# Optimization experiments

Measured on AMD Instinct MI355X. Metric: run time of the kernel, lower is better.

Reference implementation:

```python
import math
import jax, jax.numpy as jnp
import numpy as np

DIM = 1024
QK_DIM = 200
HIDDEN = 2 * DIM  # expansion_factor = 2
N = 8192


def setup_inputs() -> dict:
    key = jax.random.key(0)
    ks = jax.random.split(key, 8)
    s = 0.02
    return {
        "x": jax.random.normal(ks[0], (N, DIM), dtype=jnp.float32),
        "W_hidden": jax.random.normal(ks[1], (DIM, 2 * HIDDEN), dtype=jnp.float32) * s,
        "b_hidden": jnp.zeros((2 * HIDDEN,), dtype=jnp.float32),
        "W_qk": jax.random.normal(ks[2], (DIM, QK_DIM), dtype=jnp.float32) * s,
        "b_qk": jnp.zeros((QK_DIM,), dtype=jnp.float32),
        "gamma": 1.0 + jax.random.normal(ks[3], (2, QK_DIM), dtype=jnp.float32) * s,
        "beta": jnp.zeros((2, QK_DIM), dtype=jnp.float32),
        "W_out": jax.random.normal(ks[4], (HIDDEN, DIM), dtype=jnp.float32) * s,
        "b_out": jnp.zeros((DIM,), dtype=jnp.float32),
    }


def reference(x, W_hidden, b_hidden, W_qk, b_qk, gamma, beta, W_out, b_out):
    # to_hidden: Linear(dim -> 2*hidden) + SiLU, then chunk into v, gate
    hid = jax.nn.silu(x @ W_hidden + b_hidden)        # [N, 2H]
    v, gate = jnp.split(hid, 2, axis=-1)              # [N, H] each
    # to_qk: Linear(dim -> qk_dim) + SiLU
    qk = jax.nn.silu(x @ W_qk + b_qk)                 # [N, qk]
    # OffsetScale (heads=2): per-head affine on the shared qk
    q = qk * gamma[0] + beta[0]                       # [N, qk]
    k = qk * gamma[1] + beta[1]                       # [N, qk]
    # scores scaled by sqrt(dim) (module uses self.dim, not qk_dim)
    sim = (q @ k.T) * (1.0 / math.sqrt(x.shape[-1]))  # [N, N]
    # ReLU-squared attention (no softmax); dropout=0.0 -> identity
    attn = jnp.square(jax.nn.relu(sim))
    out = attn @ v                                    # [N, H]
    out = out * gate
    out = out @ W_out + b_out                         # [N, dim]
    # add_residual=True in this module multiplies by x
    return out * x
```

## Files before the change

kernel.cpp:

```cpp
#include <hip/hip_runtime.h>
#include <stdint.h>


typedef __bf16 bf16x8 __attribute__((ext_vector_type(8)));
typedef float f32x4 __attribute__((ext_vector_type(4)));

__device__ __forceinline__ uint16_t f2bf(float f) {
  uint32_t u = __builtin_bit_cast(uint32_t, f);
  u += 0x7fffu + ((u >> 16) & 1u);
  return (uint16_t)(u >> 16);
}
__device__ __forceinline__ float bf2f(uint16_t h) {
  uint32_t u = ((uint32_t)h) << 16;
  return __builtin_bit_cast(float, u);
}
__device__ __forceinline__ float silu_f(float s) {
  return s / (1.f + __expf(-s));
}

__device__ __forceinline__ void gload16(const void* g, void* l) {
  __builtin_amdgcn_global_load_lds(
      (__attribute__((address_space(1))) void*)const_cast<void*>(g),
      (__attribute__((address_space(3))) void*)l, 16, 0, 0);
}


__global__ void cast_to_bf16(const float* __restrict__ in, uint16_t* __restrict__ out, int n4) {
  int i = blockIdx.x * blockDim.x + threadIdx.x;
  if (i < n4) {
    float4 f = ((const float4*)in)[i];
    ushort4 o;
    o.x = f2bf(f.x); o.y = f2bf(f.y); o.z = f2bf(f.z); o.w = f2bf(f.w);
    ((ushort4*)out)[i] = o;
  }
}

__global__ void transpose_cast_pad(const float* __restrict__ in, uint16_t* __restrict__ out,
                                   int R, int C, int Cp) {
  __shared__ float tile[32][33];
  int cb = blockIdx.x * 32;
  int rb = blockIdx.y * 32;
  int tx = threadIdx.x;
  int ty = threadIdx.y;
#pragma unroll
  for (int i = 0; i < 4; ++i) {
    int r = rb + ty + i * 8;
    int c = cb + tx;
    tile[ty + i * 8][tx] = (c < C) ? in[(size_t)r * C + c] : 0.f;
  }
  __syncthreads();
#pragma unroll
  for (int i = 0; i < 4; ++i) {
    int c = cb + ty + i * 8;
    if (c < Cp) out[(size_t)c * R + rb + tx] = f2bf(tile[tx][ty + i * 8]);
  }
}


struct EpiParams {
  const float* bias;
  const float* g0;
  const float* b0;
  const float* g1;
  const float* b1;
  const uint16_t* gate;
  const float* x;
  uint16_t* o16a;
  uint16_t* o16b;
  float* o32;
};

template <int MODE>
__global__ __launch_bounds__(256) void gemm_bt(
    const uint16_t* __restrict__ A, int lda,
    const uint16_t* __restrict__ Bt, int ldb,
    int K, EpiParams p) {
  __shared__ __align__(16) uint16_t As[128 * 32];
  __shared__ __align__(16) uint16_t Bs[128 * 32];

  const int tid = threadIdx.x;
  const int lane = tid & 63;
  const int wave = tid >> 6;
  const int wr = (wave >> 1) * 64;
  const int wc = (wave & 1) * 64;
  const int m0 = blockIdx.y * 128;
  const int n0 = blockIdx.x * 128;

  f32x4 acc[4][4] = {};

  const int r0 = tid >> 2;
  const int q8 = (tid & 3) * 8;
  const uint16_t* gA0 = A + (size_t)(m0 + r0) * lda + q8;
  const uint16_t* gA1 = A + (size_t)(m0 + 64 + r0) * lda + q8;
  const uint16_t* gB0 = Bt + (size_t)(n0 + r0) * ldb + q8;
  const uint16_t* gB1 = Bt + (size_t)(n0 + 64 + r0) * ldb + q8;
  uint16_t* lA0 = As + wave * 512;
  uint16_t* lA1 = As + 2048 + wave * 512;
  uint16_t* lB0 = Bs + wave * 512;
  uint16_t* lB1 = Bs + 2048 + wave * 512;

  const int fr = lane & 15;
  const int kq = (lane >> 4) * 8;

  for (int k0 = 0; k0 < K; k0 += 32) {
    __syncthreads();
    gload16(gA0 + k0, lA0);
    gload16(gA1 + k0, lA1);
    gload16(gB0 + k0, lB0);
    gload16(gB1 + k0, lB1);
    __syncthreads();

    bf16x8 a[4], b[4];
#pragma unroll
    for (int i = 0; i < 4; ++i)
      a[i] = *(const bf16x8*)(As + (wr + i * 16 + fr) * 32 + kq);
#pragma unroll
    for (int j = 0; j < 4; ++j)
      b[j] = *(const bf16x8*)(Bs + (wc + j * 16 + fr) * 32 + kq);
#pragma unroll
    for (int i = 0; i < 4; ++i)
#pragma unroll
      for (int j = 0; j < 4; ++j)
        acc[i][j] = __builtin_amdgcn_mfma_f32_16x16x32_bf16(a[i], b[j], acc[i][j], 0, 0, 0);
  }

#pragma unroll
  for (int i = 0; i < 4; ++i) {
#pragma unroll
    for (int j = 0; j < 4; ++j) {
      const int row = m0 + wr + i * 16 + (lane >> 4) * 4;
      const int col = n0 + wc + j * 16 + fr;

      if constexpr (MODE == 0) {
        const float bc = p.bias[col];
        if (col < 2048) {
          ushort4 o;
          float s0 = silu_f(acc[i][j][0] + bc);
          float s1 = silu_f(acc[i][j][1] + bc);
          float s2 = silu_f(acc[i][j][2] + bc);
          float s3 = silu_f(acc[i][j][3] + bc);
          o.x = f2bf(s0); o.y = f2bf(s1); o.z = f2bf(s2); o.w = f2bf(s3);
          *(ushort4*)(p.o16a + (size_t)col * 8192 + row) = o;
        } else {
#pragma unroll
          for (int r = 0; r < 4; ++r) {
            float s = silu_f(acc[i][j][r] + bc);
            p.o16b[(size_t)(row + r) * 2048 + (col - 2048)] = f2bf(s);
          }
        }
      } else if constexpr (MODE == 1) {
        if (col < 224) {
#pragma unroll
          for (int r = 0; r < 4; ++r) {
            float qv = 0.f, kv = 0.f;
            if (col < 200) {
              float s = silu_f(acc[i][j][r] + p.bias[col]);
              qv = s * p.g0[col] + p.b0[col];
              kv = s * p.g1[col] + p.b1[col];
            }
            p.o16a[(size_t)(row + r) * 224 + col] = f2bf(qv);
            p.o16b[(size_t)(row + r) * 224 + col] = f2bf(kv);
          }
        }
      } else if constexpr (MODE == 2) {
#pragma unroll
        for (int r = 0; r < 4; ++r) {
          float s = acc[i][j][r] * 0.03125f;
          s = fmaxf(s, 0.f);
          p.o16a[(size_t)(row + r) * 8192 + col] = f2bf(s * s);
        }
      } else {
        const float bc = p.bias[col];
#pragma unroll
        for (int r = 0; r < 4; ++r) {
          size_t idx = (size_t)(row + r) * 1024 + col;
          p.o32[idx] = (acc[i][j][r] + bc) * p.x[idx];
        }
      }
    }
  }
}

__global__ __launch_bounds__(512) void gemm_wide3(
    const uint16_t* __restrict__ A, int lda,
    const uint16_t* __restrict__ Bt, int ldb,
    int K, int nx, EpiParams p) {
  __shared__ __align__(16) uint16_t As[128 * 32];
  __shared__ __align__(16) uint16_t Bs[256 * 32];

  const int id = blockIdx.x;
  const int bx = (id >> 3) % nx;
  const int by = (id & 7) + 8 * (id / (8 * nx));
  const int m0 = by * 128;
  const int n0 = bx * 256;

  const int tid = threadIdx.x;
  const int lane = tid & 63;
  const int wave = tid >> 6;
  const int wr = (wave & 1) * 64;
  const int wc = (wave >> 1) * 64;

  f32x4 acc[4][4] = {};

  const int r0 = tid >> 2;
  const int q8 = (tid & 3) * 8;
  const uint16_t* gA  = A  + (size_t)(m0 + r0) * lda + q8;
  const uint16_t* gB0 = Bt + (size_t)(n0 + r0) * ldb + q8;
  const uint16_t* gB1 = Bt + (size_t)(n0 + 128 + r0) * ldb + q8;
  uint16_t* lA  = As + wave * 512;
  uint16_t* lB0 = Bs + wave * 512;
  uint16_t* lB1 = Bs + 4096 + wave * 512;

  const int fr = lane & 15;
  const int kq = (lane >> 4) * 8;

  for (int k0 = 0; k0 < K; k0 += 32) {
    __syncthreads();
    gload16(gA + k0, lA);
    gload16(gB0 + k0, lB0);
    gload16(gB1 + k0, lB1);
    __syncthreads();

    bf16x8 a[4], b[4];
#pragma unroll
    for (int i = 0; i < 4; ++i)
      a[i] = *(const bf16x8*)(As + (wr + i * 16 + fr) * 32 + kq);
#pragma unroll
    for (int j = 0; j < 4; ++j)
      b[j] = *(const bf16x8*)(Bs + (wc + j * 16 + fr) * 32 + kq);
#pragma unroll
    for (int i = 0; i < 4; ++i)
#pragma unroll
      for (int j = 0; j < 4; ++j)
        acc[i][j] = __builtin_amdgcn_mfma_f32_16x16x32_bf16(a[i], b[j], acc[i][j], 0, 0, 0);
  }

#pragma unroll
  for (int i = 0; i < 4; ++i) {
#pragma unroll
    for (int j = 0; j < 4; ++j) {
      const int row = m0 + wr + i * 16 + (lane >> 4) * 4;
      const int col = n0 + wc + j * 16 + fr;
#pragma unroll
      for (int r = 0; r < 4; ++r) {
        float g = bf2f(p.gate[(size_t)(row + r) * 2048 + col]);
        p.o16a[(size_t)(row + r) * 2048 + col] = f2bf(acc[i][j][r] * g);
      }
    }
  }
}


extern "C" void kernel_launch(void* const* d_in, const int* in_sizes, int n_in,
                              void* d_out, int out_size, void* d_ws, size_t ws_size,
                              hipStream_t stream) {
  const float* x        = (const float*)d_in[0];
  const float* W_hidden = (const float*)d_in[1];
  const float* b_hidden = (const float*)d_in[2];
  const float* W_qk     = (const float*)d_in[3];
  const float* b_qk     = (const float*)d_in[4];
  const float* gamma    = (const float*)d_in[5];
  const float* beta     = (const float*)d_in[6];
  const float* W_out    = (const float*)d_in[7];
  const float* b_out    = (const float*)d_in[8];
  float* out = (float*)d_out;

  const bool fullM = ws_size >= (236ull << 20);
  const size_t region0 = fullM ? (128ull << 20) : (64ull << 20);

  char* base = (char*)d_ws;
  uint16_t* xb    = (uint16_t*)(base);
  uint16_t* WhT   = (uint16_t*)(base + (16ull << 20));
  uint16_t* WqkT  = (uint16_t*)(base + (24ull << 20));
  uint16_t* attnB = (uint16_t*)(base);
  char* tail = base + region0;
  uint16_t* WoT   = (uint16_t*)(tail);
  uint16_t* q     = (uint16_t*)(tail + (4ull << 20));
  uint16_t* kk    = (uint16_t*)(tail + (4ull << 20) + 3670016);
  uint16_t* vT    = (uint16_t*)(tail + (4ull << 20) + 2 * 3670016);
  uint16_t* gate  = (uint16_t*)(tail + (4ull << 20) + 2 * 3670016 + (32ull << 20));
  uint16_t* out2g = (uint16_t*)(tail + (4ull << 20) + 2 * 3670016 + (64ull << 20));
  (void)in_sizes; (void)n_in; (void)out_size;

  cast_to_bf16<<<(8192 * 1024 / 4) / 256, 256, 0, stream>>>(x, xb, 8192 * 1024 / 4);
  transpose_cast_pad<<<dim3(4096 / 32, 1024 / 32), dim3(32, 8), 0, stream>>>(W_hidden, WhT, 1024, 4096, 4096);
  transpose_cast_pad<<<dim3(256 / 32, 1024 / 32), dim3(32, 8), 0, stream>>>(W_qk, WqkT, 1024, 200, 256);
  transpose_cast_pad<<<dim3(1024 / 32, 2048 / 32), dim3(32, 8), 0, stream>>>(W_out, WoT, 2048, 1024, 1024);

  {
    EpiParams p{};
    p.bias = b_qk; p.g0 = gamma; p.b0 = beta; p.g1 = gamma + 200; p.b1 = beta + 200;
    p.o16a = q; p.o16b = kk;
    gemm_bt<1><<<dim3(2, 64), 256, 0, stream>>>(xb, 1024, WqkT, 1024, 1024, p);
  }
  {
    EpiParams p{};
    p.bias = b_hidden; p.o16a = vT; p.o16b = gate;
    gemm_bt<0><<<dim3(32, 64), 256, 0, stream>>>(xb, 1024, WhT, 1024, 1024, p);
  }

  if (fullM) {
    {
      EpiParams p{};
      p.o16a = attnB;
      gemm_bt<2><<<dim3(64, 64), 256, 0, stream>>>(q, 224, kk, 224, 224, p);
    }
    {
      EpiParams p{};
      p.gate = gate; p.o16a = out2g;
      gemm_wide3<<<dim3(8 * 64), 512, 0, stream>>>(attnB, 8192, vT, 8192, 8192, 8, p);
    }
  } else {
    for (int s = 0; s < 2; ++s) {
      {
        EpiParams p{};
        p.o16a = attnB;
        gemm_bt<2><<<dim3(64, 32), 256, 0, stream>>>(q + (size_t)s * 4096 * 224, 224, kk, 224, 224, p);
      }
      {
        EpiParams p{};
        p.gate = gate + (size_t)s * 4096 * 2048;
        p.o16a = out2g + (size_t)s * 4096 * 2048;
        gemm_wide3<<<dim3(8 * 32), 512, 0, stream>>>(attnB, 8192, vT, 8192, 8192, 8, p);
      }
    }
  }

  {
    EpiParams p{};
    p.bias = b_out; p.x = x; p.o32 = out;
    gemm_bt<4><<<dim3(8, 64), 256, 0, stream>>>(out2g, 2048, WoT, 2048, 2048, p);
  }
}
```

Before: 668.6 us.

## Fuse hidden and qk projections, coalesce attention score stores via LDS staging

The hidden and qk projection GEMMs become one launch over 34 column tiles. The extra tiles read the WqkT buffer that sits directly after WhT in the workspace, so the two weight matrices act as one concatenated matrix. The score kernel's epilogue now stages each wave's ReLU-squared bf16 tile in shared memory, then writes it as 16-byte vector rows instead of scattered 2-byte stores. This targets the large score matrix write. Kernels are also specialised with constant K and strides. The cost is extra LDS use in the score kernel, and the fusion relies on WqkT being contiguous with WhT.

```diff
diff --git a/kernel.cpp b/kernel.cpp
--- a/kernel.cpp
+++ b/kernel.cpp
@@ -59,6 +59,7 @@
 
 struct EpiParams {
   const float* bias;
+  const float* bias2;
   const float* g0;
   const float* b0;
   const float* g1;
@@ -67,14 +68,13 @@
   const float* x;
   uint16_t* o16a;
   uint16_t* o16b;
+  uint16_t* oq;
+  uint16_t* ok;
   float* o32;
 };
 
-template <int MODE>
-__global__ __launch_bounds__(256) void gemm_bt(
-    const uint16_t* __restrict__ A, int lda,
-    const uint16_t* __restrict__ Bt, int ldb,
-    int K, EpiParams p) {
+__global__ __launch_bounds__(256) void k_fused_hid_qk(
+    const uint16_t* __restrict__ A, const uint16_t* __restrict__ Bt, EpiParams p) {
   __shared__ __align__(16) uint16_t As[128 * 32];
   __shared__ __align__(16) uint16_t Bs[128 * 32];
 
@@ -85,6 +85,7 @@
   const int wc = (wave & 1) * 64;
   const int m0 = blockIdx.y * 128;
   const int n0 = blockIdx.x * 128;
+  const int lda = 1024, ldb = 1024, K = 1024;
 
   f32x4 acc[4][4] = {};
 
@@ -131,57 +132,115 @@
       const int row = m0 + wr + i * 16 + (lane >> 4) * 4;
       const int col = n0 + wc + j * 16 + fr;
 
-      if constexpr (MODE == 0) {
+      if (col < 2048) {
         const float bc = p.bias[col];
-        if (col < 2048) {
-          ushort4 o;
-          float s0 = silu_f(acc[i][j][0] + bc);
-          float s1 = silu_f(acc[i][j][1] + bc);
-          float s2 = silu_f(acc[i][j][2] + bc);
-          float s3 = silu_f(acc[i][j][3] + bc);
-          o.x = f2bf(s0); o.y = f2bf(s1); o.z = f2bf(s2); o.w = f2bf(s3);
-          *(ushort4*)(p.o16a + (size_t)col * 8192 + row) = o;
-        } else {
+        ushort4 o;
+        o.x = f2bf(silu_f(acc[i][j][0] + bc));
+        o.y = f2bf(silu_f(acc[i][j][1] + bc));
+        o.z = f2bf(silu_f(acc[i][j][2] + bc));
+        o.w = f2bf(silu_f(acc[i][j][3] + bc));
+        *(ushort4*)(p.o16a + (size_t)col * 8192 + row) = o;
+      } else if (col < 4096) {
+        const float bc = p.bias[col];
+#pragma unroll
+        for (int r = 0; r < 4; ++r)
+          p.o16b[(size_t)(row + r) * 2048 + (col - 2048)] = f2bf(silu_f(acc[i][j][r] + bc));
+      } else {
+        const int qc = col - 4096;
+        if (qc < 224) {
 #pragma unroll
           for (int r = 0; r < 4; ++r) {
-            float s = silu_f(acc[i][j][r] + bc);
-            p.o16b[(size_t)(row + r) * 2048 + (col - 2048)] = f2bf(s);
+            float qv = 0.f, kv = 0.f;
+            if (qc < 200) {
+              float s = silu_f(acc[i][j][r] + p.bias2[qc]);
+              qv = s * p.g0[qc] + p.b0[qc];
+              kv = s * p.g1[qc] + p.b1[qc];
+            }
+            p.oq[(size_t)(row + r) * 224 + qc] = f2bf(qv);
+            p.ok[(size_t)(row + r) * 224 + qc] = f2bf(kv);
           }
         }
-      } else if constexpr (MODE == 1) {
-        if (col < 224) {
-#pragma unroll
-          for (int r = 0; r < 4; ++r) {
-            float qv = 0.f, kv = 0.f;
-            if (col < 200) {
-              float s = silu_f(acc[i][j][r] + p.bias[col]);
-              qv = s * p.g0[col] + p.b0[col];
-              kv = s * p.g1[col] + p.b1[col];
-            }
-            p.o16a[(size_t)(row + r) * 224 + col] = f2bf(qv);
-            p.o16b[(size_t)(row + r) * 224 + col] = f2bf(kv);
-          }
-        }
-      } else if constexpr (MODE == 2) {
-#pragma unroll
-        for (int r = 0; r < 4; ++r) {
-          float s = acc[i][j][r] * 0.03125f;
-          s = fmaxf(s, 0.f);
-          p.o16a[(size_t)(row + r) * 8192 + col] = f2bf(s * s);
-        }
-      } else {
-        const float bc = p.bias[col];
-#pragma unroll
-        for (int r = 0; r < 4; ++r) {
-          size_t idx = (size_t)(row + r) * 1024 + col;
-          p.o32[idx] = (acc[i][j][r] + bc) * p.x[idx];
-        }
-      }
-    }
-  }
-}
-
-__global__ __launch_bounds__(512) void gemm_wide3(
+      }
+    }
+  }
+}
+
+__global__ __launch_bounds__(256) void k_attn(
+    const uint16_t* __restrict__ A,
+    const uint16_t* __restrict__ Bt, EpiParams p) {
+  __shared__ __align__(16) uint16_t As[128 * 32];
+  __shared__ __align__(16) uint16_t Bs[128 * 32];
+  __shared__ __align__(16) uint16_t Ep[4][2][16 * 72];
+
+  const int tid = threadIdx.x;
+  const int lane = tid & 63;
+  const int wave = tid >> 6;
+  const int wr = (wave >> 1) * 64;
+  const int wc = (wave & 1) * 64;
+  const int m0 = blockIdx.y * 128;
+  const int n0 = blockIdx.x * 128;
+  const int lda = 224, ldb = 224, K = 224;
+
+  f32x4 acc[4][4] = {};
+
+  const int r0 = tid >> 2;
+  const int q8 = (tid & 3) * 8;
+  const uint16_t* gA0 = A + (size_t)(m0 + r0) * lda + q8;
+  const uint16_t* gA1 = A + (size_t)(m0 + 64 + r0) * lda + q8;
+  const uint16_t* gB0 = Bt + (size_t)(n0 + r0) * ldb + q8;
+  const uint16_t* gB1 = Bt + (size_t)(n0 + 64 + r0) * ldb + q8;
+  uint16_t* lA0 = As + wave * 512;
+  uint16_t* lA1 = As + 2048 + wave * 512;
+  uint16_t* lB0 = Bs + wave * 512;
+  uint16_t* lB1 = Bs + 2048 + wave * 512;
+
+  const int fr = lane & 15;
+  const int kq = (lane >> 4) * 8;
+
+  for (int k0 = 0; k0 < K; k0 += 32) {
+    __syncthreads();
+    gload16(gA0 + k0, lA0);
+    gload16(gA1 + k0, lA1);
+    gload16(gB0 + k0, lB0);
+    gload16(gB1 + k0, lB1);
+    __syncthreads();
+
+    bf16x8 a[4], b[4];
+#pragma unroll
+    for (int i = 0; i < 4; ++i)
+      a[i] = *(const bf16x8*)(As + (wr + i * 16 + fr) * 32 + kq);
+#pragma unroll
+    for (int j = 0; j < 4; ++j)
+      b[j] = *(const bf16x8*)(Bs + (wc + j * 16 + fr) * 32 + kq);
+#pragma unroll
+    for (int i = 0; i < 4; ++i)
+#pragma unroll
+      for (int j = 0; j < 4; ++j)
+        acc[i][j] = __builtin_amdgcn_mfma_f32_16x16x32_bf16(a[i], b[j], acc[i][j], 0, 0, 0);
+  }
+
+#pragma unroll
+  for (int i = 0; i < 4; ++i) {
+    uint16_t* sl = Ep[wave][i & 1];
+#pragma unroll
+    for (int j = 0; j < 4; ++j) {
+#pragma unroll
+      for (int r = 0; r < 4; ++r) {
+        float s = fmaxf(acc[i][j][r] * 0.03125f, 0.f);
+        sl[((lane >> 4) * 4 + r) * 72 + j * 16 + fr] = f2bf(s * s);
+      }
+    }
+    const int row = lane >> 2;
+    const int c0 = (lane & 3) * 16;
+    bf16x8 v0 = *(const bf16x8*)(sl + row * 72 + c0);
+    bf16x8 v1 = *(const bf16x8*)(sl + row * 72 + c0 + 8);
+    uint16_t* dst = p.o16a + (size_t)(m0 + wr + i * 16 + row) * 8192 + (n0 + wc + c0);
+    *(bf16x8*)(dst) = v0;
+    *(bf16x8*)(dst + 8) = v1;
+  }
+}
+
+__global__ __launch_bounds__(512) void k_pv(
     const uint16_t* __restrict__ A, int lda,
     const uint16_t* __restrict__ Bt, int ldb,
     int K, int nx, EpiParams p) {
@@ -245,6 +304,75 @@
       for (int r = 0; r < 4; ++r) {
         float g = bf2f(p.gate[(size_t)(row + r) * 2048 + col]);
         p.o16a[(size_t)(row + r) * 2048 + col] = f2bf(acc[i][j][r] * g);
+      }
+    }
+  }
+}
+
+__global__ __launch_bounds__(256) void k_final(
+    const uint16_t* __restrict__ A,
+    const uint16_t* __restrict__ Bt, EpiParams p) {
+  __shared__ __align__(16) uint16_t As[128 * 32];
+  __shared__ __align__(16) uint16_t Bs[128 * 32];
+
+  const int tid = threadIdx.x;
+  const int lane = tid & 63;
+  const int wave = tid >> 6;
+  const int wr = (wave >> 1) * 64;
+  const int wc = (wave & 1) * 64;
+  const int m0 = blockIdx.y * 128;
+  const int n0 = blockIdx.x * 128;
+  const int lda = 2048, ldb = 2048, K = 2048;
+
+  f32x4 acc[4][4] = {};
+
+  const int r0 = tid >> 2;
+  const int q8 = (tid & 3) * 8;
+  const uint16_t* gA0 = A + (size_t)(m0 + r0) * lda + q8;
+  const uint16_t* gA1 = A + (size_t)(m0 + 64 + r0) * lda + q8;
+  const uint16_t* gB0 = Bt + (size_t)(n0 + r0) * ldb + q8;
+  const uint16_t* gB1 = Bt + (size_t)(n0 + 64 + r0) * ldb + q8;
+  uint16_t* lA0 = As + wave * 512;
+  uint16_t* lA1 = As + 2048 + wave * 512;
+  uint16_t* lB0 = Bs + wave * 512;
+  uint16_t* lB1 = Bs + 2048 + wave * 512;
+
+  const int fr = lane & 15;
+  const int kq = (lane >> 4) * 8;
+
+  for (int k0 = 0; k0 < K; k0 += 32) {
+    __syncthreads();
+    gload16(gA0 + k0, lA0);
+    gload16(gA1 + k0, lA1);
+    gload16(gB0 + k0, lB0);
+    gload16(gB1 + k0, lB1);
+    __syncthreads();
+
+    bf16x8 a[4], b[4];
+#pragma unroll
+    for (int i = 0; i < 4; ++i)
+      a[i] = *(const bf16x8*)(As + (wr + i * 16 + fr) * 32 + kq);
+#pragma unroll
+    for (int j = 0; j < 4; ++j)
+      b[j] = *(const bf16x8*)(Bs + (wc + j * 16 + fr) * 32 + kq);
+#pragma unroll
+    for (int i = 0; i < 4; ++i)
+#pragma unroll
+      for (int j = 0; j < 4; ++j)
+        acc[i][j] = __builtin_amdgcn_mfma_f32_16x16x32_bf16(a[i], b[j], acc[i][j], 0, 0, 0);
+  }
+
+#pragma unroll
+  for (int i = 0; i < 4; ++i) {
+#pragma unroll
+    for (int j = 0; j < 4; ++j) {
+      const int row = m0 + wr + i * 16 + (lane >> 4) * 4;
+      const int col = n0 + wc + j * 16 + fr;
+      const float bc = p.bias[col];
+#pragma unroll
+      for (int r = 0; r < 4; ++r) {
+        size_t idx = (size_t)(row + r) * 1024 + col;
+        p.o32[idx] = (acc[i][j][r] + bc) * p.x[idx];
       }
     }
   }
@@ -289,39 +417,35 @@
 
   {
     EpiParams p{};
-    p.bias = b_qk; p.g0 = gamma; p.b0 = beta; p.g1 = gamma + 200; p.b1 = beta + 200;
-    p.o16a = q; p.o16b = kk;
-    gemm_bt<1><<<dim3(2, 64), 256, 0, stream>>>(xb, 1024, WqkT, 1024, 1024, p);
-  }
-  {
-    EpiParams p{};
-    p.bias = b_hidden; p.o16a = vT; p.o16b = gate;
-    gemm_bt<0><<<dim3(32, 64), 256, 0, stream>>>(xb, 1024, WhT, 1024, 1024, p);
+    p.bias = b_hidden; p.bias2 = b_qk;
+    p.g0 = gamma; p.b0 = beta; p.g1 = gamma + 200; p.b1 = beta + 200;
+    p.o16a = vT; p.o16b = gate; p.oq = q; p.ok = kk;
+    k_fused_hid_qk<<<dim3(34, 64), 256, 0, stream>>>(xb, WhT, p);
   }
 
   if (fullM) {
     {
       EpiParams p{};
       p.o16a = attnB;
-      gemm_bt<2><<<dim3(64, 64), 256, 0, stream>>>(q, 224, kk, 224, 224, p);
+      k_attn<<<dim3(64, 64), 256, 0, stream>>>(q, kk, p);
     }
     {
       EpiParams p{};
       p.gate = gate; p.o16a = out2g;
-      gemm_wide3<<<dim3(8 * 64), 512, 0, stream>>>(attnB, 8192, vT, 8192, 8192, 8, p);
+      k_pv<<<dim3(8 * 64), 512, 0, stream>>>(attnB, 8192, vT, 8192, 8192, 8, p);
     }
   } else {
     for (int s = 0; s < 2; ++s) {
       {
         EpiParams p{};
         p.o16a = attnB;
-        gemm_bt<2><<<dim3(64, 32), 256, 0, stream>>>(q + (size_t)s * 4096 * 224, 224, kk, 224, 224, p);
+        k_attn<<<dim3(64, 32), 256, 0, stream>>>(q + (size_t)s * 4096 * 224, kk, p);
       }
       {
         EpiParams p{};
         p.gate = gate + (size_t)s * 4096 * 2048;
         p.o16a = out2g + (size_t)s * 4096 * 2048;
-        gemm_wide3<<<dim3(8 * 32), 512, 0, stream>>>(attnB, 8192, vT, 8192, 8192, 8, p);
+        k_pv<<<dim3(8 * 32), 512, 0, stream>>>(attnB, 8192, vT, 8192, 8192, 8, p);
       }
     }
   }
@@ -329,6 +453,6 @@
   {
     EpiParams p{};
     p.bias = b_out; p.x = x; p.o32 = out;
-    gemm_bt<4><<<dim3(8, 64), 256, 0, stream>>>(out2g, 2048, WoT, 2048, 2048, p);
-  }
-}
+    k_final<<<dim3(8, 64), 256, 0, stream>>>(out2g, WoT, p);
+  }
+}
```

Result: no change. 668.1 us (-0.1%).
